# Kernel tuning notes

Hardware: AMD Instinct MI355X
Metric: run time of the kernel (lower is better)

The kernel has to match this reference:

```python
import jax, jax.numpy as jnp
import numpy as np

BATCH = 8192
INPUT_DIM = 10240
NODES = 1024          # == INPUT_DIM // 10, required by compressed @ adjacency
ACTIONS = 64
HIDDEN = 128
BINS = 100
HLO, HHI = -5.0, 5.0
ENTROPY_THRESH = 2.5


def _semantic_mask(n):
    m = np.zeros((n, n), dtype=np.float32)
    m[9, 0] = 1.0; m[9, 1] = 1.0; m[3, 0] = 1.0; m[2, 7] = 1.0; m[6, 4] = 1.0
    np.fill_diagonal(m, 1.0)
    m[8, 5] = 1.0; m[8, 1] = 1.0; m[8, 3] = 1.0
    if n > 6:
        m[5, 6] = 10.0
        m[1, 6] = 5.0
    if n > 5:
        m[5, 3] = 2.0
    return jnp.asarray(m)


def setup_inputs() -> dict:
    key = jax.random.key(0)
    ks = jax.random.split(key, 6)
    event_stream = jax.random.normal(ks[0], (BATCH, INPUT_DIM), dtype=jnp.float32)
    sensing_matrix = jax.random.normal(ks[1], (INPUT_DIM // 10, INPUT_DIM), dtype=jnp.float32)
    # adjacency is a trainable parameter (zeros at init); use small random values
    # so the downstream state/policy computation is non-degenerate.
    adjacency = 0.01 * jax.random.normal(ks[2], (NODES, NODES), dtype=jnp.float32)
    semantic_mask = _semantic_mask(NODES)
    W1 = jax.random.normal(ks[3], (HIDDEN, NODES), dtype=jnp.float32) / np.sqrt(NODES)
    b1 = jnp.zeros((HIDDEN,), dtype=jnp.float32)
    W2 = jax.random.normal(ks[4], (ACTIONS, HIDDEN), dtype=jnp.float32) / np.sqrt(HIDDEN)
    b2 = jnp.zeros((ACTIONS,), dtype=jnp.float32)
    return {"event_stream": event_stream, "sensing_matrix": sensing_matrix,
            "adjacency": adjacency, "semantic_mask": semantic_mask,
            "W1": W1, "b1": b1, "W2": W2, "b2": b2}


def _batched_histc(x):
    # Faithful vectorized torch.histc(bins=100, min=-5, max=5):
    # out-of-range values are ignored; values == max land in the last bin.
    b = x.shape[0]
    idx = jnp.clip(jnp.floor((x - HLO) / (HHI - HLO) * BINS).astype(jnp.int32), 0, BINS - 1)
    in_range = ((x >= HLO) & (x <= HHI)).astype(x.dtype)
    rows = jnp.broadcast_to(jnp.arange(b)[:, None], x.shape)
    return jnp.zeros((b, BINS), dtype=x.dtype).at[rows, idx].add(in_range)


def _policy(s, W1, b1, W2, b2):
    h = jax.nn.relu(s @ W1.T + b1)
    return h @ W2.T + b2


def reference(event_stream, sensing_matrix, adjacency, semantic_mask, W1, b1, W2, b2):
    # --- Layer 1: information filter (batched histogram + Shannon entropy gate) ---
    hist = _batched_histc(event_stream)                       # [B, 100]
    prob = hist / (hist.sum(-1, keepdims=True) + 1e-9)
    h_ent = -(prob * jnp.log(prob + 1e-9)).sum(-1)            # [B]
    compressed = event_stream @ sensing_matrix.T              # [B, NODES]
    keep = (h_ent >= ENTROPY_THRESH)[:, None].astype(compressed.dtype)
    filtered = compressed * keep                              # zeros where low entropy

    # --- Layer 2: causal forward ---
    state = filtered @ adjacency                              # [B, NODES]

    # --- Semantic consistency loss ---
    semantic_loss = jnp.sum(jnp.abs(adjacency) * semantic_mask)

    # --- Layer 3: robust Nash policy (training path: sign-grad perturbation) ---
    grad_s = jax.grad(lambda s: _policy(s, W1, b1, W2, b2).mean())(state)
    perturbation = jnp.sign(grad_s)
    robust_logits = _policy(state - 0.1 * perturbation, W1, b1, W2, b2)
    action_probs = jax.nn.softmax(robust_logits, axis=-1)     # [B, ACTIONS]

    return action_probs, adjacency, semantic_loss
```

## Files before the change

kernel.cpp:

```cpp
#include <hip/hip_runtime.h>
#include <hip/hip_bf16.h>

typedef unsigned short u16;
typedef short v8s __attribute__((ext_vector_type(8)));
typedef float v4f __attribute__((ext_vector_type(4)));

#define BATCH 8192
#define IND 10240
#define NODES 1024
#define ACTIONS 64
#define HIDDEN 128

__device__ __forceinline__ u16 f2b(float x) {
    __hip_bfloat16 h = __float2bfloat16(x);
    return *reinterpret_cast<u16*>(&h);
}

__device__ __forceinline__ float b2f(u16 x) {
    unsigned u = ((unsigned)x) << 16;
    return *reinterpret_cast<float*>(&u);
}

__device__ __forceinline__ void gload16(const void* g, void* l) {
    __builtin_amdgcn_global_load_lds(
        (const __attribute__((address_space(1))) void*)g,
        (__attribute__((address_space(3))) void*)l, 16, 0, 0);
}

#define SBAR() do { __builtin_amdgcn_s_barrier(); \
                    __builtin_amdgcn_sched_barrier(0); } while (0)
#define VMCNT4() asm volatile("s_waitcnt vmcnt(4)" ::: "memory")
#define VMCNT0() asm volatile("s_waitcnt vmcnt(0)" ::: "memory")

__global__ __launch_bounds__(256) void hist_entropy_cast(
    const float* __restrict__ E, u16* __restrict__ Ebf, float* __restrict__ keep)
{
    __shared__ int hist[4][100];
    const int tid = threadIdx.x;
    const int wave = tid >> 6;
    const int b = blockIdx.x;
    for (int j = tid; j < 400; j += 256) ((int*)hist)[j] = 0;
    __syncthreads();

    const float* row = E + (size_t)b * IND;
    u16* orow = Ebf + (size_t)b * IND;
    for (int i = tid * 4; i < IND; i += 1024) {
        float4 v = *reinterpret_cast<const float4*>(row + i);
        float xs[4] = {v.x, v.y, v.z, v.w};
        u16 ob[4];
#pragma unroll
        for (int j = 0; j < 4; ++j) {
            float x = xs[j];
            ob[j] = f2b(x);
            if (x >= -5.0f && x <= 5.0f) {
                int idx = (int)floorf((x + 5.0f) / 10.0f * 100.0f);
                idx = idx < 0 ? 0 : (idx > 99 ? 99 : idx);
                atomicAdd(&hist[wave][idx], 1);
            }
        }
        u16 packed[4] = {ob[0], ob[1], ob[2], ob[3]};
        *reinterpret_cast<uint2*>(orow + i) = *reinterpret_cast<uint2*>(packed);
    }
    __syncthreads();
    if (tid < 100)
        hist[0][tid] = hist[0][tid] + hist[1][tid] + hist[2][tid] + hist[3][tid];
    __syncthreads();

    if (tid < 64) {
        float c0 = (float)hist[0][tid];
        float c1 = (tid < 36) ? (float)hist[0][tid + 64] : 0.0f;
        float tot = c0 + c1;
#pragma unroll
        for (int s = 32; s >= 1; s >>= 1) tot += __shfl_xor(tot, s);
        float denom = tot + 1e-9f;
        float p0 = c0 / denom, p1 = c1 / denom;
        float e = -(p0 * logf(p0 + 1e-9f)) - (p1 * logf(p1 + 1e-9f));
#pragma unroll
        for (int s = 32; s >= 1; s >>= 1) e += __shfl_xor(e, s);
        if (tid == 0) keep[b] = (e >= 2.5f) ? 1.0f : 0.0f;
    }
}

__global__ __launch_bounds__(256) void cvt_bf16(
    const float* __restrict__ in, u16* __restrict__ out, long n4)
{
    long i = (long)blockIdx.x * blockDim.x + threadIdx.x;
    const long stride = (long)gridDim.x * blockDim.x;
    for (; i < n4; i += stride) {
        float4 v = reinterpret_cast<const float4*>(in)[i];
        u16 o[4] = {f2b(v.x), f2b(v.y), f2b(v.z), f2b(v.w)};
        reinterpret_cast<uint2*>(out)[i] = *reinterpret_cast<uint2*>(o);
    }
}

__global__ void transpose_cvt(const float* __restrict__ in, u16* __restrict__ out,
                              int R, int C)
{
    __shared__ float t[32][33];
    const int bx = blockIdx.x * 32, by = blockIdx.y * 32;
    const int tx = threadIdx.x, ty = threadIdx.y;
#pragma unroll
    for (int j = 0; j < 32; j += 8) {
        int r = by + ty + j, c = bx + tx;
        if (r < R && c < C) t[ty + j][tx] = in[(size_t)r * C + c];
    }
    __syncthreads();
#pragma unroll
    for (int j = 0; j < 32; j += 8) {
        int oc = by + tx;
        int orow = bx + ty + j;
        if (orow < C && oc < R) out[(size_t)orow * R + oc] = f2b(t[tx][ty + j]);
    }
}

__global__ void w2sum_k(const float* __restrict__ W2, float* __restrict__ w2s)
{
    int i = threadIdx.x;
    if (i < HIDDEN) {
        float s = 0.f;
        for (int a = 0; a < ACTIONS; ++a) s += W2[a * HIDDEN + i];
        w2s[i] = s;
    }
}

__global__ __launch_bounds__(256) void semloss1(
    const float* __restrict__ A, const float* __restrict__ M, float* __restrict__ part)
{
    const int tid = threadIdx.x;
    float s = 0.f;
    for (int i = blockIdx.x * 256 + tid; i < NODES * NODES; i += 256 * gridDim.x)
        s += fabsf(A[i]) * M[i];
    __shared__ float ws[4];
#pragma unroll
    for (int off = 32; off >= 1; off >>= 1) s += __shfl_xor(s, off);
    if ((tid & 63) == 0) ws[tid >> 6] = s;
    __syncthreads();
    if (tid == 0) part[blockIdx.x] = ws[0] + ws[1] + ws[2] + ws[3];
}

__global__ void semloss2(const float* __restrict__ part, float* __restrict__ out, int n)
{
    const int tid = threadIdx.x;
    float s = (tid < n) ? part[tid] : 0.f;
    __shared__ float ws[4];
#pragma unroll
    for (int off = 32; off >= 1; off >>= 1) s += __shfl_xor(s, off);
    if ((tid & 63) == 0) ws[tid >> 6] = s;
    __syncthreads();
    if (tid == 0) out[0] = ws[0] + ws[1] + ws[2] + ws[3];
}

__global__ __launch_bounds__(256) void combine_keep(
    const float* __restrict__ p0, const float* __restrict__ p1,
    const float* __restrict__ keep, u16* __restrict__ filt)
{
    long base = ((long)blockIdx.x * 256 + threadIdx.x) * 4;
    float4 a = *reinterpret_cast<const float4*>(p0 + base);
    float4 b = *reinterpret_cast<const float4*>(p1 + base);
    float k = keep[base >> 10];
    u16 o[4] = {f2b((a.x + b.x) * k), f2b((a.y + b.y) * k),
                f2b((a.z + b.z) * k), f2b((a.w + b.w) * k)};
    *reinterpret_cast<uint2*>(filt + base) = *reinterpret_cast<uint2*>(o);
}

__device__ __forceinline__ void stage_chunk(
    const u16* __restrict__ g, char* lds, int chunk_off, int kt_col,
    int tid, int wave)
{
    const int s_row0 = tid >> 2;
    const int gblk = (tid & 3) ^ ((tid >> 3) & 3);
#pragma unroll
    for (int j = 0; j < 2; ++j) {
        int lrow = j * 128 + s_row0;
        gload16(g + (size_t)lrow * IND + kt_col + (gblk << 3),
                lds + chunk_off + j * 8192 + (wave << 10));
    }
}

__global__ __launch_bounds__(512, 2) void gemm8_ep0(
    const u16* __restrict__ A, const u16* __restrict__ B,
    float* __restrict__ outf)
{
    extern __shared__ char lds[];
    const int tid = threadIdx.x;
    const int wave = tid >> 6, lane = tid & 63;
    const int wr = wave >> 2, wcn = wave & 3;
    const int l15 = lane & 15, lhi = lane >> 4;
    const int rsw = (lhi ^ ((l15 >> 1) & 3)) << 4;
    const size_t koff = (size_t)blockIdx.z * (IND / 2);
    const u16* Ag = A + (size_t)(blockIdx.x * 256) * IND + koff;
    const u16* Bg = B + (size_t)(blockIdx.y * 256) * IND + koff;

    v4f acc[8][4];
#pragma unroll
    for (int m = 0; m < 8; ++m)
#pragma unroll
        for (int n = 0; n < 4; ++n) acc[m][n] = (v4f){0.f, 0.f, 0.f, 0.f};

    v8s a[8], b0, b1;
    const int arow = wr * 128 * 64;
    const int brow0 = wcn * 64 * 64;

#define LDA(P, KS, M) (*reinterpret_cast<const v8s*>( \
    lds + ((P)*2 + (KS)) * 16384 + arow + ((M)*16 + l15) * 64 + rsw))
#define LDB(P, KS, NF) (*reinterpret_cast<const v8s*>( \
    lds + 65536 + ((P)*2 + (KS)) * 16384 + brow0 + ((NF)*16 + l15) * 64 + rsw))
#define MFMA2(NH) do { \
    _Pragma("unroll") \
    for (int m = 0; m < 8; ++m) { \
        acc[m][2*(NH)]   = __builtin_amdgcn_mfma_f32_16x16x32_bf16( \
            a[m], b0, acc[m][2*(NH)], 0, 0, 0); \
        acc[m][2*(NH)+1] = __builtin_amdgcn_mfma_f32_16x16x32_bf16( \
            a[m], b1, acc[m][2*(NH)+1], 0, 0, 0); \
    } } while (0)

#define TILE(P, KTN, STG) do { \
     \
    _Pragma("unroll") \
    for (int m = 0; m < 8; ++m) a[m] = LDA(P, 0, m); \
    b0 = LDB(P, 0, 0); b1 = LDB(P, 0, 1); \
    if (STG) stage_chunk(Ag, lds, ((P^1)*2 + 0) * 16384, (KTN), tid, wave); \
    SBAR(); \
    __builtin_amdgcn_s_setprio(1); MFMA2(0); __builtin_amdgcn_s_setprio(0); \
    SBAR(); \
     \
    b0 = LDB(P, 0, 2); b1 = LDB(P, 0, 3); \
    if (STG) { stage_chunk(Bg, lds, 65536 + ((P^1)*2 + 0) * 16384, (KTN), tid, wave); \
               VMCNT4(); } else { VMCNT0(); } \
    SBAR(); \
    __builtin_amdgcn_s_setprio(1); MFMA2(1); __builtin_amdgcn_s_setprio(0); \
    SBAR(); \
     \
    _Pragma("unroll") \
    for (int m = 0; m < 8; ++m) a[m] = LDA(P, 1, m); \
    b0 = LDB(P, 1, 0); b1 = LDB(P, 1, 1); \
    if (STG) stage_chunk(Ag, lds, ((P^1)*2 + 1) * 16384, (KTN) + 32, tid, wave); \
    SBAR(); \
    __builtin_amdgcn_s_setprio(1); MFMA2(0); __builtin_amdgcn_s_setprio(0); \
    SBAR(); \
     \
    b0 = LDB(P, 1, 2); b1 = LDB(P, 1, 3); \
    if (STG) { stage_chunk(Bg, lds, 65536 + ((P^1)*2 + 1) * 16384, (KTN) + 32, tid, wave); \
               VMCNT4(); } \
    SBAR(); \
    __builtin_amdgcn_s_setprio(1); MFMA2(1); __builtin_amdgcn_s_setprio(0); \
    SBAR(); \
} while (0)

    stage_chunk(Ag, lds, 0 * 16384, 0, tid, wave);
    stage_chunk(Bg, lds, 65536 + 0 * 16384, 0, tid, wave);
    stage_chunk(Ag, lds, 1 * 16384, 32, tid, wave);
    stage_chunk(Bg, lds, 65536 + 1 * 16384, 32, tid, wave);
    VMCNT4();
    SBAR();

#pragma unroll 1
    for (int tp = 0; tp < 39; ++tp) {
        TILE(0, (2 * tp + 1) * 64, 1);
        TILE(1, (2 * tp + 2) * 64, 1);
    }
    TILE(0, 79 * 64, 1);
    TILE(1, 0, 0);

#undef TILE
#undef MFMA2
#undef LDB
#undef LDA

    const size_t zo = (size_t)blockIdx.z * ((size_t)BATCH * NODES);
    const int grow0 = blockIdx.x * 256 + wr * 128 + (lhi << 2);
    const int gcol0 = blockIdx.y * 256 + wcn * 64 + l15;
#pragma unroll
    for (int m = 0; m < 8; ++m)
#pragma unroll
        for (int n = 0; n < 4; ++n)
#pragma unroll
            for (int j = 0; j < 4; ++j)
                outf[zo + (size_t)(grow0 + m * 16 + j) * NODES + gcol0 + n * 16] =
                    acc[m][n][j];
}

template<int EP>
__global__ __launch_bounds__(256) void gemm_bt(
    const u16* __restrict__ A, const u16* __restrict__ B, int K, int N,
    const float* __restrict__ aux0, const float* __restrict__ aux1,
    u16* __restrict__ outb)
{
    __shared__ u16 As[2][128 * 64];
    __shared__ u16 Bs[2][128 * 64];
    const int tid = threadIdx.x;
    const int wave = tid >> 6, lane = tid & 63;
    const int wr = wave >> 1, wc = wave & 1;
    const int l15 = lane & 15, lhi = lane >> 4;
    const int swz = (l15 & 7) << 3;
    const int src_c = (((lane & 7) ^ (lane >> 3)) << 3);
    const int src_r = lane >> 3;
    const u16* Ag = A + (size_t)(blockIdx.x * 128) * K;
    const u16* Bg = B + (size_t)(blockIdx.y * 128) * K;

    v4f acc[4][4];
#pragma unroll
    for (int m = 0; m < 4; ++m)
#pragma unroll
        for (int n = 0; n < 4; ++n) acc[m][n] = (v4f){0.f, 0.f, 0.f, 0.f};

#pragma unroll
    for (int i = 0; i < 4; ++i) {
        int chunk = wave * 4 + i;
        int r = chunk * 8 + src_r;
        gload16(Ag + (size_t)r * K + src_c, &As[0][chunk * 512]);
        gload16(Bg + (size_t)r * K + src_c, &Bs[0][chunk * 512]);
    }
    __syncthreads();

    int cur = 0;
    for (int kt = 0; kt < K; kt += 64) {
        if (kt + 64 < K) {
            int nxt = cur ^ 1;
#pragma unroll
            for (int i = 0; i < 4; ++i) {
                int chunk = wave * 4 + i;
                int r = chunk * 8 + src_r;
                gload16(Ag + (size_t)r * K + (kt + 64 + src_c), &As[nxt][chunk * 512]);
                gload16(Bg + (size_t)r * K + (kt + 64 + src_c), &Bs[nxt][chunk * 512]);
            }
        }
#pragma unroll
        for (int ks = 0; ks < 2; ++ks) {
            v8s a[4], b[4];
#pragma unroll
            for (int m = 0; m < 4; ++m)
                a[m] = *reinterpret_cast<const v8s*>(
                    &As[cur][(wr * 64 + m * 16 + l15) * 64 + ((ks * 32 + (lhi << 3)) ^ swz)]);
#pragma unroll
            for (int n = 0; n < 4; ++n)
                b[n] = *reinterpret_cast<const v8s*>(
                    &Bs[cur][(wc * 64 + n * 16 + l15) * 64 + ((ks * 32 + (lhi << 3)) ^ swz)]);
#pragma unroll
            for (int m = 0; m < 4; ++m)
#pragma unroll
                for (int n = 0; n < 4; ++n)
                    acc[m][n] = __builtin_amdgcn_mfma_f32_16x16x32_bf16(
                        a[m], b[n], acc[m][n], 0, 0, 0);
        }
        __syncthreads();
        cur ^= 1;
    }

    const int m0 = blockIdx.x * 128 + wr * 64;
    const int n0 = blockIdx.y * 128 + wc * 64;
#pragma unroll
    for (int m = 0; m < 4; ++m) {
#pragma unroll
        for (int j = 0; j < 4; ++j) {
            int row = m0 + m * 16 + (lhi << 2) + j;
#pragma unroll
            for (int n = 0; n < 4; ++n) {
                int col = n0 + n * 16 + l15;
                float v = acc[m][n][j];
                size_t off = (size_t)row * N + col;
                if (EP == 1) {
                    outb[off] = f2b(v);
                } else if (EP == 2) {
                    float h = v + aux0[col];
                    outb[off] = (h > 0.f) ? f2b(aux1[col]) : (u16)0;
                } else {
                    float sg = (v > 0.f) ? 1.f : ((v < 0.f) ? -1.f : 0.f);
                    float sv = b2f(((const u16*)aux0)[off]);
                    outb[off] = f2b(sv - 0.1f * sg);
                }
            }
        }
    }
}

__global__ __launch_bounds__(256) void policy_final(
    const u16* __restrict__ S2, const u16* __restrict__ W1b,
    const float* __restrict__ b1, const u16* __restrict__ W2b,
    const float* __restrict__ b2, float* __restrict__ probs)
{
    __shared__ u16 As[128 * 64];
    __shared__ u16 Bs[128 * 64];
    __shared__ u16 H2[128 * 128];
    const int tid = threadIdx.x;
    const int wave = tid >> 6, lane = tid & 63;
    const int wr = wave >> 1, wc = wave & 1;
    const int l15 = lane & 15, lhi = lane >> 4;
    const int swz = (l15 & 7) << 3;
    const int src_c = (((lane & 7) ^ (lane >> 3)) << 3);
    const int src_r = lane >> 3;
    const u16* Ag = S2 + (size_t)(blockIdx.x * 128) * NODES;

    v4f acc[4][4];
#pragma unroll
    for (int m = 0; m < 4; ++m)
#pragma unroll
        for (int n = 0; n < 4; ++n) acc[m][n] = (v4f){0.f, 0.f, 0.f, 0.f};

    for (int kt = 0; kt < NODES; kt += 64) {
#pragma unroll
        for (int i = 0; i < 4; ++i) {
            int chunk = wave * 4 + i;
            int r = chunk * 8 + src_r;
            gload16(Ag + (size_t)r * NODES + (kt + src_c), &As[chunk * 512]);
            gload16(W1b + (size_t)r * NODES + (kt + src_c), &Bs[chunk * 512]);
        }
        __syncthreads();
#pragma unroll
        for (int ks = 0; ks < 2; ++ks) {
            v8s a[4], b[4];
#pragma unroll
            for (int m = 0; m < 4; ++m)
                a[m] = *reinterpret_cast<const v8s*>(
                    &As[(wr * 64 + m * 16 + l15) * 64 + ((ks * 32 + (lhi << 3)) ^ swz)]);
#pragma unroll
            for (int n = 0; n < 4; ++n)
                b[n] = *reinterpret_cast<const v8s*>(
                    &Bs[(wc * 64 + n * 16 + l15) * 64 + ((ks * 32 + (lhi << 3)) ^ swz)]);
#pragma unroll
            for (int m = 0; m < 4; ++m)
#pragma unroll
                for (int n = 0; n < 4; ++n)
                    acc[m][n] = __builtin_amdgcn_mfma_f32_16x16x32_bf16(
                        a[m], b[n], acc[m][n], 0, 0, 0);
        }
        __syncthreads();
    }

#pragma unroll
    for (int m = 0; m < 4; ++m)
#pragma unroll
        for (int j = 0; j < 4; ++j) {
            int lrow = wr * 64 + m * 16 + (lhi << 2) + j;
#pragma unroll
            for (int n = 0; n < 4; ++n) {
                int col = wc * 64 + n * 16 + l15;
                float v = acc[m][n][j] + b1[col];
                H2[lrow * 128 + (col ^ ((lrow & 7) << 3))] = f2b(v > 0.f ? v : 0.f);
            }
        }
#pragma unroll
    for (int i = 0; i < 4; ++i) {
        int e = (tid + i * 256) * 8;
        int row = e >> 7, col = e & 127;
        int dst = (row << 7) | (col ^ ((row & 7) << 3));
        *reinterpret_cast<v8s*>(&Bs[dst]) = *reinterpret_cast<const v8s*>(&W2b[e]);
    }
    __syncthreads();

    v4f a2[2][4];
#pragma unroll
    for (int m = 0; m < 2; ++m)
#pragma unroll
        for (int n = 0; n < 4; ++n) a2[m][n] = (v4f){0.f, 0.f, 0.f, 0.f};
#pragma unroll
    for (int ks = 0; ks < 4; ++ks) {
        v8s af[2], bf[4];
#pragma unroll
        for (int m = 0; m < 2; ++m)
            af[m] = *reinterpret_cast<const v8s*>(
                &H2[(wave * 32 + m * 16 + l15) * 128 + ((ks * 32 + (lhi << 3)) ^ swz)]);
#pragma unroll
        for (int n = 0; n < 4; ++n)
            bf[n] = *reinterpret_cast<const v8s*>(
                &Bs[(n * 16 + l15) * 128 + ((ks * 32 + (lhi << 3)) ^ swz)]);
#pragma unroll
        for (int m = 0; m < 2; ++m)
#pragma unroll
            for (int n = 0; n < 4; ++n)
                a2[m][n] = __builtin_amdgcn_mfma_f32_16x16x32_bf16(
                    af[m], bf[n], a2[m][n], 0, 0, 0);
    }

#pragma unroll
    for (int m = 0; m < 2; ++m) {
#pragma unroll
        for (int j = 0; j < 4; ++j) {
            int lrow = wave * 32 + m * 16 + (lhi << 2) + j;
            float v[4];
#pragma unroll
            for (int n = 0; n < 4; ++n) v[n] = a2[m][n][j] + b2[n * 16 + l15];
            float mx = fmaxf(fmaxf(v[0], v[1]), fmaxf(v[2], v[3]));
#pragma unroll
            for (int s = 8; s >= 1; s >>= 1) mx = fmaxf(mx, __shfl_xor(mx, s));
            float e[4], sum = 0.f;
#pragma unroll
            for (int n = 0; n < 4; ++n) { e[n] = expf(v[n] - mx); sum += e[n]; }
#pragma unroll
            for (int s = 8; s >= 1; s >>= 1) sum += __shfl_xor(sum, s);
            float inv = 1.0f / sum;
            size_t base = (size_t)(blockIdx.x * 128 + lrow) * ACTIONS;
#pragma unroll
            for (int n = 0; n < 4; ++n) probs[base + n * 16 + l15] = e[n] * inv;
        }
    }
}

extern "C" void kernel_launch(void* const* d_in, const int* in_sizes, int n_in,
                              void* d_out, int out_size, void* d_ws, size_t ws_size,
                              hipStream_t stream)
{
    const float* E   = (const float*)d_in[0];
    const float* S   = (const float*)d_in[1];
    const float* Adj = (const float*)d_in[2];
    const float* Msk = (const float*)d_in[3];
    const float* W1  = (const float*)d_in[4];
    const float* b1  = (const float*)d_in[5];
    const float* W2  = (const float*)d_in[6];
    const float* b2  = (const float*)d_in[7];
    float* out = (float*)d_out;

    char* ws = (char*)d_ws;
    u16*  Ebf  = (u16*)  (ws + 0UL);
    u16*  Sbf  = (u16*)  (ws + 167772160UL);
    u16*  Atb  = (u16*)  (ws + 188743680UL);
    u16*  W1b  = (u16*)  (ws + 190840832UL);
    u16*  W1tb = (u16*)  (ws + 191102976UL);
    u16*  W2b  = (u16*)  (ws + 191365120UL);
    float* w2s = (float*)(ws + 191381504UL);
    float* keep= (float*)(ws + 191382016UL);
    float* part= (float*)(ws + 191414784UL);
    u16*  filt = (u16*)  (ws + 191415808UL);
    float* pbuf = (float*)(ws + 208193024UL);
    u16*  stb  = (u16*)  (ws + 208193024UL);
    u16*  dbuf = (u16*)  (ws + 224970240UL);
    u16*  s2   = (u16*)  (ws + 227067392UL);

    hipFuncSetAttribute((const void*)gemm8_ep0,
                        hipFuncAttributeMaxDynamicSharedMemorySize, 131072);

    dim3 tb(32, 8);
    hist_entropy_cast<<<8192, 256, 0, stream>>>(E, Ebf, keep);
    cvt_bf16<<<2048, 256, 0, stream>>>(S, Sbf, (long)NODES * IND / 4);
    cvt_bf16<<<128, 256, 0, stream>>>(W1, W1b, (long)HIDDEN * NODES / 4);
    cvt_bf16<<<8, 256, 0, stream>>>(W2, W2b, (long)ACTIONS * HIDDEN / 4);
    transpose_cvt<<<dim3(32, 32), tb, 0, stream>>>(Adj, Atb, NODES, NODES);
    transpose_cvt<<<dim3(32, 4),  tb, 0, stream>>>(W1, W1tb, HIDDEN, NODES);
    w2sum_k<<<1, 128, 0, stream>>>(W2, w2s);
    semloss1<<<256, 256, 0, stream>>>(Adj, Msk, part);
    semloss2<<<1, 256, 0, stream>>>(part, out + 524288 + 1048576, 256);
    hipMemcpyAsync(out + 524288, Adj, sizeof(float) * 1048576,
                   hipMemcpyDeviceToDevice, stream);

    gemm8_ep0<<<dim3(32, 4, 2), 512, 131072, stream>>>(Ebf, Sbf, pbuf);
    combine_keep<<<8192, 256, 0, stream>>>(pbuf, pbuf + (size_t)BATCH * NODES,
                                           keep, filt);
    gemm_bt<1><<<dim3(64, 8), 256, 0, stream>>>(filt, Atb, NODES, NODES,
                                                nullptr, nullptr, stb);
    gemm_bt<2><<<dim3(64, 1), 256, 0, stream>>>(stb, W1b, NODES, HIDDEN,
                                                b1, w2s, dbuf);
    gemm_bt<3><<<dim3(64, 8), 256, 0, stream>>>(dbuf, W1tb, HIDDEN, NODES,
                                                (const float*)stb, nullptr, s2);
    policy_final<<<64, 256, 0, stream>>>(s2, W1b, b1, W2b, b2, out);
}
```

Measured before the change: 388.1 us.

## Double-buffer MFMA operand registers to overlap LDS reads with matrix math

The main split-K GEMM loop now keeps two sets of A and B fragment registers. Each phase issues the LDS reads for the next phase while the current phase's MFMAs run on already-loaded fragments, and the next tile's first fragments are prefetched at the end of each tile. The global-to-LDS staging of the A and B chunks is also grouped into single points per half-tile. This aims to hide LDS read latency behind MFMA work, at the cost of more vector registers and some risk of lower occupancy or spills.

```diff
diff --git a/kernel.cpp b/kernel.cpp
--- a/kernel.cpp
+++ b/kernel.cpp
@@ -197,7 +197,7 @@
 #pragma unroll
         for (int n = 0; n < 4; ++n) acc[m][n] = (v4f){0.f, 0.f, 0.f, 0.f};
 
-    v8s a[8], b0, b1;
+    v8s axA[8], axB[8], bx0, bx1, by0, by1;
     const int arow = wr * 128 * 64;
     const int brow0 = wcn * 64 * 64;
 
@@ -205,45 +205,51 @@
     lds + ((P)*2 + (KS)) * 16384 + arow + ((M)*16 + l15) * 64 + rsw))
 #define LDB(P, KS, NF) (*reinterpret_cast<const v8s*>( \
     lds + 65536 + ((P)*2 + (KS)) * 16384 + brow0 + ((NF)*16 + l15) * 64 + rsw))
-#define MFMA2(NH) do { \
+#define MFMA8(AR, B0, B1, NH) do { \
     _Pragma("unroll") \
     for (int m = 0; m < 8; ++m) { \
         acc[m][2*(NH)]   = __builtin_amdgcn_mfma_f32_16x16x32_bf16( \
-            a[m], b0, acc[m][2*(NH)], 0, 0, 0); \
+            AR[m], B0, acc[m][2*(NH)], 0, 0, 0); \
         acc[m][2*(NH)+1] = __builtin_amdgcn_mfma_f32_16x16x32_bf16( \
-            a[m], b1, acc[m][2*(NH)+1], 0, 0, 0); \
+            AR[m], B1, acc[m][2*(NH)+1], 0, 0, 0); \
     } } while (0)
 
 #define TILE(P, KTN, STG) do { \
      \
-    _Pragma("unroll") \
-    for (int m = 0; m < 8; ++m) a[m] = LDA(P, 0, m); \
-    b0 = LDB(P, 0, 0); b1 = LDB(P, 0, 1); \
-    if (STG) stage_chunk(Ag, lds, ((P^1)*2 + 0) * 16384, (KTN), tid, wave); \
-    SBAR(); \
-    __builtin_amdgcn_s_setprio(1); MFMA2(0); __builtin_amdgcn_s_setprio(0); \
-    SBAR(); \
-     \
-    b0 = LDB(P, 0, 2); b1 = LDB(P, 0, 3); \
-    if (STG) { stage_chunk(Bg, lds, 65536 + ((P^1)*2 + 0) * 16384, (KTN), tid, wave); \
-               VMCNT4(); } else { VMCNT0(); } \
-    SBAR(); \
-    __builtin_amdgcn_s_setprio(1); MFMA2(1); __builtin_amdgcn_s_setprio(0); \
+    by0 = LDB(P, 0, 2); by1 = LDB(P, 0, 3); \
+    if (STG) { \
+        stage_chunk(Ag, lds, ((P^1)*2 + 0) * 16384, (KTN), tid, wave); \
+        stage_chunk(Bg, lds, 65536 + ((P^1)*2 + 0) * 16384, (KTN), tid, wave); \
+        VMCNT4(); \
+    } else { VMCNT0(); } \
+    SBAR(); \
+    __builtin_amdgcn_s_setprio(1); MFMA8(axA, bx0, bx1, 0); __builtin_amdgcn_s_setprio(0); \
     SBAR(); \
      \
     _Pragma("unroll") \
-    for (int m = 0; m < 8; ++m) a[m] = LDA(P, 1, m); \
-    b0 = LDB(P, 1, 0); b1 = LDB(P, 1, 1); \
-    if (STG) stage_chunk(Ag, lds, ((P^1)*2 + 1) * 16384, (KTN) + 32, tid, wave); \
-    SBAR(); \
-    __builtin_amdgcn_s_setprio(1); MFMA2(0); __builtin_amdgcn_s_setprio(0); \
+    for (int m = 0; m < 8; ++m) axB[m] = LDA(P, 1, m); \
+    bx0 = LDB(P, 1, 0); bx1 = LDB(P, 1, 1); \
+    SBAR(); \
+    __builtin_amdgcn_s_setprio(1); MFMA8(axA, by0, by1, 1); __builtin_amdgcn_s_setprio(0); \
     SBAR(); \
      \
-    b0 = LDB(P, 1, 2); b1 = LDB(P, 1, 3); \
-    if (STG) { stage_chunk(Bg, lds, 65536 + ((P^1)*2 + 1) * 16384, (KTN) + 32, tid, wave); \
-               VMCNT4(); } \
-    SBAR(); \
-    __builtin_amdgcn_s_setprio(1); MFMA2(1); __builtin_amdgcn_s_setprio(0); \
+    by0 = LDB(P, 1, 2); by1 = LDB(P, 1, 3); \
+    if (STG) { \
+        stage_chunk(Ag, lds, ((P^1)*2 + 1) * 16384, (KTN) + 32, tid, wave); \
+        stage_chunk(Bg, lds, 65536 + ((P^1)*2 + 1) * 16384, (KTN) + 32, tid, wave); \
+        VMCNT4(); \
+    } \
+    SBAR(); \
+    __builtin_amdgcn_s_setprio(1); MFMA8(axB, bx0, bx1, 0); __builtin_amdgcn_s_setprio(0); \
+    SBAR(); \
+     \
+    if (STG) { \
+        _Pragma("unroll") \
+        for (int m = 0; m < 8; ++m) axA[m] = LDA(P^1, 0, m); \
+        bx0 = LDB(P^1, 0, 0); bx1 = LDB(P^1, 0, 1); \
+    } \
+    SBAR(); \
+    __builtin_amdgcn_s_setprio(1); MFMA8(axB, by0, by1, 1); __builtin_amdgcn_s_setprio(0); \
     SBAR(); \
 } while (0)
 
@@ -253,6 +259,9 @@
     stage_chunk(Bg, lds, 65536 + 1 * 16384, 32, tid, wave);
     VMCNT4();
     SBAR();
+#pragma unroll
+    for (int m = 0; m < 8; ++m) axA[m] = LDA(0, 0, m);
+    bx0 = LDB(0, 0, 0); bx1 = LDB(0, 0, 1);
 
 #pragma unroll 1
     for (int tp = 0; tp < 39; ++tp) {
@@ -263,7 +272,7 @@
     TILE(1, 0, 0);
 
 #undef TILE
-#undef MFMA2
+#undef MFMA8
 #undef LDB
 #undef LDA
 
```

New measurement: 400.6 us. 3.2% more time.

## Load A operand directly from global into registers, stage only B through LDS

Applied to the files above, without the earlier changes.

The main compression GEMM now loads the A (event stream) fragments straight from global memory into double-buffered registers, and only B (sensing matrix) goes through a four-slot LDS ring. This halves LDS usage, cutting dynamic shared memory from 128KB to 64KB, and removes the LDS write and read traffic for A. In exchange, each wave issues uncoalesced-ish 16-byte global loads per row, with no sharing of A between the four column waves. That multiplies A global/L2 traffic and adds register pressure.

```diff
diff --git a/kernel.cpp b/kernel.cpp
--- a/kernel.cpp
+++ b/kernel.cpp
@@ -29,8 +29,9 @@
 
 #define SBAR() do { __builtin_amdgcn_s_barrier(); \
                     __builtin_amdgcn_sched_barrier(0); } while (0)
-#define VMCNT4() asm volatile("s_waitcnt vmcnt(4)" ::: "memory")
-#define VMCNT0() asm volatile("s_waitcnt vmcnt(0)" ::: "memory")
+#define VMCNT10() asm volatile("s_waitcnt vmcnt(10)" ::: "memory")
+#define VMCNT8()  asm volatile("s_waitcnt vmcnt(8)" ::: "memory")
+#define VMCNT0()  asm volatile("s_waitcnt vmcnt(0)" ::: "memory")
 
 __global__ __launch_bounds__(256) void hist_entropy_cast(
     const float* __restrict__ E, u16* __restrict__ Ebf, float* __restrict__ keep)
@@ -163,18 +164,15 @@
     *reinterpret_cast<uint2*>(filt + base) = *reinterpret_cast<uint2*>(o);
 }
 
-__device__ __forceinline__ void stage_chunk(
-    const u16* __restrict__ g, char* lds, int chunk_off, int kt_col,
-    int tid, int wave)
+__device__ __forceinline__ void stage_b(
+    const u16* __restrict__ g, char* lds_slot, int col, int tid)
 {
     const int s_row0 = tid >> 2;
     const int gblk = (tid & 3) ^ ((tid >> 3) & 3);
 #pragma unroll
-    for (int j = 0; j < 2; ++j) {
-        int lrow = j * 128 + s_row0;
-        gload16(g + (size_t)lrow * IND + kt_col + (gblk << 3),
-                lds + chunk_off + j * 8192 + (wave << 10));
-    }
+    for (int j = 0; j < 2; ++j)
+        gload16(g + (size_t)(j * 128 + s_row0) * IND + col + (gblk << 3),
+                lds_slot + j * 8192 + ((tid >> 6) << 10));
 }
 
 __global__ __launch_bounds__(512, 2) void gemm8_ep0(
@@ -191,81 +189,74 @@
     const u16* Ag = A + (size_t)(blockIdx.x * 256) * IND + koff;
     const u16* Bg = B + (size_t)(blockIdx.y * 256) * IND + koff;
 
+    const u16* ap[8];
+#pragma unroll
+    for (int m = 0; m < 8; ++m)
+        ap[m] = Ag + (size_t)(wr * 128 + m * 16 + l15) * IND + (lhi << 3);
+
     v4f acc[8][4];
 #pragma unroll
     for (int m = 0; m < 8; ++m)
 #pragma unroll
         for (int n = 0; n < 4; ++n) acc[m][n] = (v4f){0.f, 0.f, 0.f, 0.f};
 
-    v8s a[8], b0, b1;
-    const int arow = wr * 128 * 64;
-    const int brow0 = wcn * 64 * 64;
-
-#define LDA(P, KS, M) (*reinterpret_cast<const v8s*>( \
-    lds + ((P)*2 + (KS)) * 16384 + arow + ((M)*16 + l15) * 64 + rsw))
-#define LDB(P, KS, NF) (*reinterpret_cast<const v8s*>( \
-    lds + 65536 + ((P)*2 + (KS)) * 16384 + brow0 + ((NF)*16 + l15) * 64 + rsw))
-#define MFMA2(NH) do { \
-    _Pragma("unroll") \
-    for (int m = 0; m < 8; ++m) { \
-        acc[m][2*(NH)]   = __builtin_amdgcn_mfma_f32_16x16x32_bf16( \
-            a[m], b0, acc[m][2*(NH)], 0, 0, 0); \
-        acc[m][2*(NH)+1] = __builtin_amdgcn_mfma_f32_16x16x32_bf16( \
-            a[m], b1, acc[m][2*(NH)+1], 0, 0, 0); \
-    } } while (0)
-
-#define TILE(P, KTN, STG) do { \
-     \
-    _Pragma("unroll") \
-    for (int m = 0; m < 8; ++m) a[m] = LDA(P, 0, m); \
-    b0 = LDB(P, 0, 0); b1 = LDB(P, 0, 1); \
-    if (STG) stage_chunk(Ag, lds, ((P^1)*2 + 0) * 16384, (KTN), tid, wave); \
+    v8s ar[2][8];
+
+#define LDB(S, NF) (*reinterpret_cast<const v8s*>( \
+    lds + (S) * 16384 + (wcn * 64 + (NF) * 16 + l15) * 64 + rsw))
+
+#define HALF(ARB, BSLOT, STSLOT, AOFS, BCOL, NISS) do { \
+    if ((NISS) >= 1) { \
+        _Pragma("unroll") \
+        for (int m = 0; m < 8; ++m) \
+            ar[(ARB)^1][m] = *reinterpret_cast<const v8s*>(ap[m] + (AOFS)); \
+    } \
+    if ((NISS) == 2) stage_b(Bg, lds + (STSLOT) * 16384, (BCOL), tid); \
+    if ((NISS) == 2) { VMCNT10(); } \
+    else if ((NISS) == 1) { VMCNT8(); } \
+    else { VMCNT0(); } \
     SBAR(); \
-    __builtin_amdgcn_s_setprio(1); MFMA2(0); __builtin_amdgcn_s_setprio(0); \
-    SBAR(); \
-     \
-    b0 = LDB(P, 0, 2); b1 = LDB(P, 0, 3); \
-    if (STG) { stage_chunk(Bg, lds, 65536 + ((P^1)*2 + 0) * 16384, (KTN), tid, wave); \
-               VMCNT4(); } else { VMCNT0(); } \
-    SBAR(); \
-    __builtin_amdgcn_s_setprio(1); MFMA2(1); __builtin_amdgcn_s_setprio(0); \
-    SBAR(); \
-     \
-    _Pragma("unroll") \
-    for (int m = 0; m < 8; ++m) a[m] = LDA(P, 1, m); \
-    b0 = LDB(P, 1, 0); b1 = LDB(P, 1, 1); \
-    if (STG) stage_chunk(Ag, lds, ((P^1)*2 + 1) * 16384, (KTN) + 32, tid, wave); \
-    SBAR(); \
-    __builtin_amdgcn_s_setprio(1); MFMA2(0); __builtin_amdgcn_s_setprio(0); \
-    SBAR(); \
-     \
-    b0 = LDB(P, 1, 2); b1 = LDB(P, 1, 3); \
-    if (STG) { stage_chunk(Bg, lds, 65536 + ((P^1)*2 + 1) * 16384, (KTN) + 32, tid, wave); \
-               VMCNT4(); } \
-    SBAR(); \
-    __builtin_amdgcn_s_setprio(1); MFMA2(1); __builtin_amdgcn_s_setprio(0); \
+    { \
+        v8s b0 = LDB(BSLOT, 0), b1 = LDB(BSLOT, 1), \
+            b2 = LDB(BSLOT, 2), b3 = LDB(BSLOT, 3); \
+        __builtin_amdgcn_s_setprio(1); \
+        _Pragma("unroll") \
+        for (int m = 0; m < 8; ++m) { \
+            acc[m][0] = __builtin_amdgcn_mfma_f32_16x16x32_bf16(ar[ARB][m], b0, acc[m][0], 0, 0, 0); \
+            acc[m][1] = __builtin_amdgcn_mfma_f32_16x16x32_bf16(ar[ARB][m], b1, acc[m][1], 0, 0, 0); \
+            acc[m][2] = __builtin_amdgcn_mfma_f32_16x16x32_bf16(ar[ARB][m], b2, acc[m][2], 0, 0, 0); \
+            acc[m][3] = __builtin_amdgcn_mfma_f32_16x16x32_bf16(ar[ARB][m], b3, acc[m][3], 0, 0, 0); \
+        } \
+        __builtin_amdgcn_s_setprio(0); \
+    } \
     SBAR(); \
 } while (0)
 
-    stage_chunk(Ag, lds, 0 * 16384, 0, tid, wave);
-    stage_chunk(Bg, lds, 65536 + 0 * 16384, 0, tid, wave);
-    stage_chunk(Ag, lds, 1 * 16384, 32, tid, wave);
-    stage_chunk(Bg, lds, 65536 + 1 * 16384, 32, tid, wave);
-    VMCNT4();
+    stage_b(Bg, lds + 0 * 16384, 0, tid);
+    stage_b(Bg, lds + 1 * 16384, 32, tid);
+#pragma unroll
+    for (int m = 0; m < 8; ++m)
+        ar[0][m] = *reinterpret_cast<const v8s*>(ap[m]);
+    VMCNT0();
     SBAR();
 
 #pragma unroll 1
-    for (int tp = 0; tp < 39; ++tp) {
-        TILE(0, (2 * tp + 1) * 64, 1);
-        TILE(1, (2 * tp + 2) * 64, 1);
-    }
-    TILE(0, 79 * 64, 1);
-    TILE(1, 0, 0);
-
-#undef TILE
-#undef MFMA2
+    for (int i = 0; i < 39; ++i) {
+        const int cb = i * 128 + 64;
+        HALF(0, 0, 2, 32,  cb,       2);
+        HALF(1, 1, 3, 64,  cb + 32,  2);
+        HALF(0, 2, 0, 96,  cb + 64,  2);
+        HALF(1, 3, 1, 128, cb + 96,  2);
+#pragma unroll
+        for (int m = 0; m < 8; ++m) ap[m] += 128;
+    }
+    HALF(0, 0, 2, 32, 158 * 32, 2);
+    HALF(1, 1, 3, 64, 159 * 32, 2);
+    HALF(0, 2, 0, 96, 0, 1);
+    HALF(1, 3, 0, 0, 0, 0);
+
+#undef HALF
 #undef LDB
-#undef LDA
 
     const size_t zo = (size_t)blockIdx.z * ((size_t)BATCH * NODES);
     const int grow0 = blockIdx.x * 256 + wr * 128 + (lhi << 2);
@@ -527,7 +518,7 @@
     u16*  s2   = (u16*)  (ws + 227067392UL);
 
     hipFuncSetAttribute((const void*)gemm8_ep0,
-                        hipFuncAttributeMaxDynamicSharedMemorySize, 131072);
+                        hipFuncAttributeMaxDynamicSharedMemorySize, 65536);
 
     dim3 tb(32, 8);
     hist_entropy_cast<<<8192, 256, 0, stream>>>(E, Ebf, keep);
@@ -542,7 +533,7 @@
     hipMemcpyAsync(out + 524288, Adj, sizeof(float) * 1048576,
                    hipMemcpyDeviceToDevice, stream);
 
-    gemm8_ep0<<<dim3(32, 4, 2), 512, 131072, stream>>>(Ebf, Sbf, pbuf);
+    gemm8_ep0<<<dim3(32, 4, 2), 512, 65536, stream>>>(Ebf, Sbf, pbuf);
     combine_keep<<<8192, 256, 0, stream>>>(pbuf, pbuf + (size_t)BATCH * NODES,
                                            keep, filt);
     gemm_bt<1><<<dim3(64, 8), 256, 0, stream>>>(filt, Atb, NODES, NODES,
```

Result: slower. 641.2 us (+65.2%).
